# Kernel optimization log

Measured on AMD Instinct MI355X. Metric: run time of the kernel, lower is better.

The kernel has to match this reference:

```python
import jax, jax.numpy as jnp
import numpy as np

B, Q, D = 4, 8, 128  # batch of volumes, poses per volume, volume side (L == D)


def setup_inputs() -> dict:
    key = jax.random.key(0)
    k1, k2 = jax.random.split(key)
    density = jax.random.normal(k1, (B, D, D, D), dtype=jnp.float32)
    rotation = jax.random.normal(k2, (B, Q, 3, 3), dtype=jnp.float32)
    return {"density": density, "rotation": rotation}


def _project(density, rotation):
    """density: (B, NZ, NY, NX); rotation: (B, Q, 3, 3) -> (B, Q, NY, NX).

    Replicates: rotate an L^3 coord grid, F.grid_sample (trilinear,
    align_corners=True, zero padding), then sum over the last grid axis.
    """
    b, NZ, NY, NX = density.shape
    q = rotation.shape[1]
    L = NZ  # module asserts D == NZ == NY == NX and uses L == D

    lin = jnp.linspace(-1.0, 1.0, L, dtype=density.dtype)
    xx, yy, zz = jnp.meshgrid(lin, lin, lin, indexing="ij")
    coords = jnp.stack([xx, yy, zz], axis=-1)  # (L, L, L, 3)

    Rf = rotation.reshape(b * q, 3, 3)
    # rot_coords[n,i,j,k,m] = sum_c coords[i,j,k,c] * R[n,c,m]
    rc = jnp.einsum("ijkc,ncm->nijkm", coords, Rf)  # (BQ, L, L, L, 3)

    # grid_sample convention: last dim is (x, y, z) indexing (NX, NY, NZ).
    # align_corners=True unnormalization: idx = (c + 1) / 2 * (size - 1)
    x = (rc[..., 0] + 1.0) * 0.5 * (NX - 1)
    y = (rc[..., 1] + 1.0) * 0.5 * (NY - 1)
    z = (rc[..., 2] + 1.0) * 0.5 * (NZ - 1)

    x0 = jnp.floor(x).astype(jnp.int32)
    y0 = jnp.floor(y).astype(jnp.int32)
    z0 = jnp.floor(z).astype(jnp.int32)
    fx = x - x0
    fy = y - y0
    fz = z - z0

    vol = jnp.broadcast_to(density[:, None], (b, q, NZ, NY, NX))
    vol_flat = vol.reshape(b * q, NZ * NY * NX)

    def corner(xc, yc, zc, w):
        valid = (xc >= 0) & (xc < NX) & (yc >= 0) & (yc < NY) & (zc >= 0) & (zc < NZ)
        xi = jnp.clip(xc, 0, NX - 1)
        yi = jnp.clip(yc, 0, NY - 1)
        zi = jnp.clip(zc, 0, NZ - 1)
        idx = (zi * NY + yi) * NX + xi  # (BQ, L, L, L)
        v = jnp.take_along_axis(vol_flat, idx.reshape(b * q, -1), axis=1)
        v = v.reshape(idx.shape)
        return jnp.where(valid, v, 0.0) * w

    sampled = (
        corner(x0,     y0,     z0,     (1 - fx) * (1 - fy) * (1 - fz))
        + corner(x0 + 1, y0,     z0,     fx * (1 - fy) * (1 - fz))
        + corner(x0,     y0 + 1, z0,     (1 - fx) * fy * (1 - fz))
        + corner(x0 + 1, y0 + 1, z0,     fx * fy * (1 - fz))
        + corner(x0,     y0,     z0 + 1, (1 - fx) * (1 - fy) * fz)
        + corner(x0 + 1, y0,     z0 + 1, fx * (1 - fy) * fz)
        + corner(x0,     y0 + 1, z0 + 1, (1 - fx) * fy * fz)
        + corner(x0 + 1, y0 + 1, z0 + 1, fx * fy * fz)
    )  # (BQ, L, L, L) over grid axes (X, Y, Z)

    sampled = sampled.reshape(b, q, L, L, L)
    proj = jnp.sum(sampled.transpose(0, 1, 3, 2, 4), axis=-1)  # (B, Q, L, L)
    return proj


def reference(density, rotation):
    return _project(density, rotation)
```

## Files before the change

### kernel.cpp

```cpp
#include <hip/hip_runtime.h>


#define LSZ 128
#define PACKED_BYTES ((size_t)4 * 128 * 128 * 128 * 8)

typedef float f2 __attribute__((ext_vector_type(2), aligned(4)));
typedef unsigned int u4v __attribute__((ext_vector_type(4), aligned(8)));

__device__ __forceinline__ float bl(unsigned int d) {
    return __uint_as_float(d << 16);
}
__device__ __forceinline__ float bh(unsigned int d) {
    return __uint_as_float(d & 0xffff0000u);
}
__device__ __forceinline__ unsigned int pk2(float lo, float hi) {
    unsigned int ul = __float_as_uint(lo), uh = __float_as_uint(hi);
    ul = (ul + 0x7fffu + ((ul >> 16) & 1u)) >> 16;
    uh = (uh + 0x7fffu + ((uh >> 16) & 1u)) >> 16;
    return ul | (uh << 16);
}

__global__ __launch_bounds__(256) void pack_kernel(
    const float* __restrict__ density, uint2* __restrict__ packed)
{
    const int t  = blockIdx.x * 256 + threadIdx.x;
    const int xq = (t & 31) << 2;
    const int y  = (t >> 5) & 127;
    const int z  = (t >> 12) & 127;
    const int b  = t >> 19;
    const float* __restrict__ v = density + ((size_t)b << 21);
    const int y1 = min(y + 1, 127), z1 = min(z + 1, 127);
    const float4 a0 = *(const float4*)(v + (z  << 14) + (y  << 7) + xq);
    const float4 a1 = *(const float4*)(v + (z  << 14) + (y1 << 7) + xq);
    const float4 c0 = *(const float4*)(v + (z1 << 14) + (y  << 7) + xq);
    const float4 c1 = *(const float4*)(v + (z1 << 14) + (y1 << 7) + xq);
    uint4 o0, o1;
    o0.x = pk2(a0.x, a1.x); o0.y = pk2(c0.x, c1.x);
    o0.z = pk2(a0.y, a1.y); o0.w = pk2(c0.y, c1.y);
    o1.x = pk2(a0.z, a1.z); o1.y = pk2(c0.z, c1.z);
    o1.z = pk2(a0.w, a1.w); o1.w = pk2(c0.w, c1.w);
    uint4* dst = (uint4*)(packed + ((size_t)b << 21) + (z << 14) + (y << 7) + xq);
    dst[0] = o0; dst[1] = o1;
}

#define FPREPI(S, kk) do {                                                    \
    const float kf_ = (float)min((kk), d);                                    \
    const float X_ = fmaf(kf_, R20, Ax);                                      \
    const float Y_ = fmaf(kf_, R21, Ay);                                      \
    const float Z_ = fmaf(kf_, R22, Az);                                      \
    const int ix_ = (int)X_;                                                  \
    const int iy_ = (int)Y_;                                                  \
    const int iz_ = (int)Z_;                                                  \
    fx##S = X_ - (float)ix_;                                                  \
    fy##S = Y_ - (float)iy_;                                                  \
    fz##S = Z_ - (float)iz_;                                                  \
    u##S = *(const u4v*)(vol2 + ((iz_ << 14) + (iy_ << 7) + ix_));            \
} while (0)

#define FCONSI(S) do {                                                        \
    const float gx0 = 1.0f - fx##S;                                           \
    const float gy0 = 1.0f - fy##S;                                           \
    const float gz0 = 1.0f - fz##S;                                           \
    const float c000 = bl(u##S.x), c010 = bh(u##S.x);                         \
    const float c001 = bl(u##S.y), c011 = bh(u##S.y);                         \
    const float c100 = bl(u##S.z), c110 = bh(u##S.z);                         \
    const float c101 = bl(u##S.w), c111 = bh(u##S.w);                         \
    const float s0_ = gy0   * fmaf(gx0, c000, fx##S * c100)                   \
                    + fy##S * fmaf(gx0, c010, fx##S * c110);                  \
    const float s1_ = gy0   * fmaf(gx0, c001, fx##S * c101)                   \
                    + fy##S * fmaf(gx0, c011, fx##S * c111);                  \
    acc = fmaf(gz0, s0_, fmaf(fz##S, s1_, acc));                              \
} while (0)

#define SPREP(S, kk) do {                                                     \
    const float kf_ = (float)(kk);                                            \
    const float X_ = fmaf(kf_, R20, Ax);                                      \
    const float Y_ = fmaf(kf_, R21, Ay);                                      \
    const float Z_ = fmaf(kf_, R22, Az);                                      \
    const int ix_ = (int)floorf(X_);                                          \
    const int iy_ = (int)floorf(Y_);                                          \
    const int iz_ = (int)floorf(Z_);                                          \
    const int ex_ = min(max(ix_, 0), 126);                                    \
    const int ey_ = min(max(iy_, 0), 126);                                    \
    const int ez_ = min(max(iz_, 0), 126);                                    \
    u##S = *(const u4v*)(vol2 + ((ez_ << 14) + (ey_ << 7) + ex_));            \
} while (0)

#define SCONS(S, kk) do {                                                     \
    const float kf_ = (float)(kk);                                            \
    const float X_ = fmaf(kf_, R20, Ax);                                      \
    const float Y_ = fmaf(kf_, R21, Ay);                                      \
    const float Z_ = fmaf(kf_, R22, Az);                                      \
    const float xf_ = floorf(X_), yf_ = floorf(Y_), zf_ = floorf(Z_);         \
    const int ix_ = (int)xf_, iy_ = (int)yf_, iz_ = (int)zf_;                 \
    const float fx_ = X_ - xf_, fy_ = Y_ - yf_, fz_ = Z_ - zf_;               \
    const bool vx0_ = (ix_ >= 0)  & (ix_ <= 127);                             \
    const bool vx1_ = (ix_ >= -1) & (ix_ <= 126);                             \
    const bool vy0_ = (iy_ >= 0)  & (iy_ <= 127);                             \
    const bool vy1_ = (iy_ >= -1) & (iy_ <= 126);                             \
    const bool vz0_ = (iz_ >= 0)  & (iz_ <= 127);                             \
    const bool vz1_ = (iz_ >= -1) & (iz_ <= 126);                             \
    const float gx0 = vx0_ ? (1.0f - fx_) : 0.0f;                             \
    const float gx1 = vx1_ ? fx_ : 0.0f;                                      \
    const float gy0 = vy0_ ? (1.0f - fy_) : 0.0f;                             \
    const float gy1 = vy1_ ? fy_ : 0.0f;                                      \
    const float gz0 = vz0_ ? (1.0f - fz_) : 0.0f;                             \
    const float gz1 = vz1_ ? fz_ : 0.0f;                                      \
    const bool xhi_ = (ix_ > 126), xlo_ = (ix_ < 0);                          \
    const bool yhi_ = (iy_ > 126), ylo_ = (iy_ < 0);                          \
    const bool zhi_ = (iz_ > 126), zlo_ = (iz_ < 0);                          \
    const unsigned int a0z0 = xhi_ ? u##S.z : u##S.x;                         \
    const unsigned int a0z1 = xhi_ ? u##S.w : u##S.y;                         \
    const unsigned int a1z0 = xlo_ ? u##S.x : u##S.z;                         \
    const unsigned int a1z1 = xlo_ ? u##S.y : u##S.w;                         \
    const unsigned int dA = zhi_ ? a0z1 : a0z0;                               \
    const unsigned int dB = zlo_ ? a0z0 : a0z1;                               \
    const unsigned int dC = zhi_ ? a1z1 : a1z0;                               \
    const unsigned int dD = zlo_ ? a1z0 : a1z1;                               \
    const float c000 = yhi_ ? bh(dA) : bl(dA);                                \
    const float c010 = ylo_ ? bl(dA) : bh(dA);                                \
    const float c100 = yhi_ ? bh(dC) : bl(dC);                                \
    const float c110 = ylo_ ? bl(dC) : bh(dC);                                \
    const float c001 = yhi_ ? bh(dB) : bl(dB);                                \
    const float c011 = ylo_ ? bl(dB) : bh(dB);                                \
    const float c101 = yhi_ ? bh(dD) : bl(dD);                                \
    const float c111 = ylo_ ? bl(dD) : bh(dD);                                \
    const float s0_ = gy0 * fmaf(gx0, c000, gx1 * c100)                       \
                    + gy1 * fmaf(gx0, c010, gx1 * c110);                      \
    const float s1_ = gy0 * fmaf(gx0, c001, gx1 * c101)                       \
                    + gy1 * fmaf(gx0, c011, gx1 * c111);                      \
    acc = fmaf(gz0, s0_, fmaf(gz1, s1_, acc));                                \
} while (0)

__global__ __launch_bounds__(256) void proj_kernel_packed(
    const uint2* __restrict__ packed,
    const float* __restrict__ rotation,
    float* __restrict__ out)
{
    const int xcd  = blockIdx.x & 7;
    const int slot = blockIdx.x >> 3;
    const int b    = xcd >> 1;
    const int tile = ((xcd & 1) << 8) + slot;
    const int q    = tile >> 6;
    const int blk  = tile & 63;
    const int bq   = (b << 3) + q;

    const int p = (blk << 8) + threadIdx.x;
    const int i = p & (LSZ - 1);
    const int j = p >> 7;

    const float* R = rotation + bq * 9;
    const float R00 = R[0], R01 = R[1], R02 = R[2];
    const float R10 = R[3], R11 = R[4], R12 = R[5];
    const float R20 = R[6], R21 = R[7], R22 = R[8];

    const float step = 2.0f / 127.0f;
    const float li = -1.0f + (float)i * step;
    const float lj = -1.0f + (float)j * step;

    const float Ax = 63.5f * (li * R00 + lj * R10 - R20 + 1.0f);
    const float Ay = 63.5f * (li * R01 + lj * R11 - R21 + 1.0f);
    const float Az = 63.5f * (li * R02 + lj * R12 - R22 + 1.0f);

    float klo = 0.0f, khi = 127.0f;
    float klo2 = 0.0f, khi2 = 127.0f;
    bool empty = false, empty2 = false;
    {
        const float a_[3] = {Ax, Ay, Az};
        const float s_[3] = {R20, R21, R22};
        #pragma unroll
        for (int m = 0; m < 3; ++m) {
            if (fabsf(s_[m]) > 1e-6f) {
                const float r = 1.0f / s_[m];
                const float t0 = (-1.0f   - a_[m]) * r;
                const float t1 = (128.0f  - a_[m]) * r;
                klo = fmaxf(klo, fminf(t0, t1));
                khi = fminf(khi, fmaxf(t0, t1));
                const float w0 = (0.0f    - a_[m]) * r;
                const float w1 = (126.95f - a_[m]) * r;
                klo2 = fmaxf(klo2, fminf(w0, w1));
                khi2 = fminf(khi2, fmaxf(w0, w1));
            } else {
                if (a_[m] <= -1.0f   || a_[m] >= 128.0f)   empty  = true;
                if (a_[m] <  0.001f  || a_[m] >  126.94f)  empty2 = true;
            }
        }
    }
    int a = (int)ceilf(klo - 1e-3f);
    int bnd = (int)floorf(khi + 1e-3f);
    if (a < 0) a = 0;
    if (bnd > 127) bnd = 127;
    if (empty) bnd = a - 1;

    int c = (int)ceilf(klo2 + 0.05f);
    int d = (int)floorf(khi2 - 0.05f);
    if (c < a) c = a;
    if (d > bnd) d = bnd;
    if (empty2 || d < c) { c = bnd + 1; d = bnd; }

    const uint2* __restrict__ vol2 = packed + ((size_t)b << 21);

    float acc = 0.0f;
    u4v uA, uB, uC, uD;
    float fxA, fyA, fzA, fxB, fyB, fzB, fxC, fyC, fzC, fxD, fyD, fzD;

    {
        int k = a;
        const int e = c - 1;
        if (k <= e) {
            SPREP(A, k);
            while (k <= e) {
                const int kn = k + 1;
                const bool hasB = (kn <= e);
                if (hasB) SPREP(B, kn);
                SCONS(A, k);
                if (hasB) SCONS(B, kn);
                k += 2;
                if (k <= e) SPREP(A, k);
            }
        }
    }

    {
        int n = d - c + 1;
        int k = c;
        if (n > 0) {
            FPREPI(A, k); FPREPI(B, k + 1); FPREPI(C, k + 2);
            while (n > 0) {
                FPREPI(D, k + 3);
                FCONSI(A);
                FPREPI(A, k + 4);
                if (n > 1) FCONSI(B);
                FPREPI(B, k + 5);
                if (n > 2) FCONSI(C);
                FPREPI(C, k + 6);
                if (n > 3) FCONSI(D);
                k += 4; n -= 4;
            }
        }
    }

    {
        int k = d + 1;
        const int e = bnd;
        if (k <= e) {
            SPREP(A, k);
            while (k <= e) {
                const int kn = k + 1;
                const bool hasB = (kn <= e);
                if (hasB) SPREP(B, kn);
                SCONS(A, k);
                if (hasB) SCONS(B, kn);
                k += 2;
                if (k <= e) SPREP(A, k);
            }
        }
    }

    out[(bq << 14) + p] = acc;
}

__global__ __launch_bounds__(256) void proj_kernel_fallback(
    const float* __restrict__ density,
    const float* __restrict__ rotation,
    float* __restrict__ out)
{
    const int xcd  = blockIdx.x & 7;
    const int slot = blockIdx.x >> 3;
    const int b    = xcd >> 1;
    const int tile = ((xcd & 1) << 8) + slot;
    const int q    = tile >> 6;
    const int blk  = tile & 63;
    const int bq   = (b << 3) + q;

    const int p = (blk << 8) + threadIdx.x;
    const int i = p & (LSZ - 1);
    const int j = p >> 7;

    const float* R = rotation + bq * 9;
    const float R00 = R[0], R01 = R[1], R02 = R[2];
    const float R10 = R[3], R11 = R[4], R12 = R[5];
    const float R20 = R[6], R21 = R[7], R22 = R[8];

    const float step = 2.0f / 127.0f;
    const float li = -1.0f + (float)i * step;
    const float lj = -1.0f + (float)j * step;

    const float Ax = 63.5f * (li * R00 + lj * R10 - R20 + 1.0f);
    const float Ay = 63.5f * (li * R01 + lj * R11 - R21 + 1.0f);
    const float Az = 63.5f * (li * R02 + lj * R12 - R22 + 1.0f);

    float klo = 0.0f, khi = 127.0f;
    bool empty = false;
    {
        const float a_[3] = {Ax, Ay, Az};
        const float s_[3] = {R20, R21, R22};
        #pragma unroll
        for (int m = 0; m < 3; ++m) {
            if (fabsf(s_[m]) > 1e-6f) {
                const float t0 = (-1.0f  - a_[m]) / s_[m];
                const float t1 = (128.0f - a_[m]) / s_[m];
                klo = fmaxf(klo, fminf(t0, t1));
                khi = fminf(khi, fmaxf(t0, t1));
            } else if (a_[m] <= -1.0f || a_[m] >= 128.0f) {
                empty = true;
            }
        }
    }
    int k_start = (int)ceilf(klo - 1e-3f);
    int k_end   = (int)floorf(khi + 1e-3f);
    if (k_start < 0) k_start = 0;
    if (k_end > 127) k_end = 127;
    if (empty) k_end = k_start - 1;

    const float* __restrict__ vol = density + (size_t)b * (LSZ * LSZ * LSZ);

    float acc = 0.0f;
    for (int k = k_start; k <= k_end; ++k) {
        const float kf = (float)k;
        const float X = fmaf(kf, R20, Ax);
        const float Y = fmaf(kf, R21, Ay);
        const float Z = fmaf(kf, R22, Az);
        const float xf = floorf(X), yf = floorf(Y), zf = floorf(Z);
        const int ix = (int)xf, iy = (int)yf, iz = (int)zf;
        const float fx = X - xf, fy = Y - yf, fz = Z - zf;
        const bool vx0 = (ix >= 0)  & (ix <= 127);
        const bool vx1 = (ix >= -1) & (ix <= 126);
        const bool vy0 = (iy >= 0)  & (iy <= 127);
        const bool vy1 = (iy >= -1) & (iy <= 126);
        const bool vz0 = (iz >= 0)  & (iz <= 127);
        const bool vz1 = (iz >= -1) & (iz <= 126);
        const int cx0 = min(max(ix, 0), 127);
        const int cx1 = min(max(ix + 1, 0), 127);
        const int cy0 = min(max(iy, 0), 127);
        const int cy1 = min(max(iy + 1, 0), 127);
        const int cz0 = min(max(iz, 0), 127);
        const int cz1 = min(max(iz + 1, 0), 127);
        const float gx0 = vx0 ? (1.0f - fx) : 0.0f;
        const float gx1 = vx1 ? fx : 0.0f;
        const float gy0 = vy0 ? (1.0f - fy) : 0.0f;
        const float gy1 = vy1 ? fy : 0.0f;
        const float gz0 = vz0 ? (1.0f - fz) : 0.0f;
        const float gz1 = vz1 ? fz : 0.0f;
        const int z0o = cz0 << 14, z1o = cz1 << 14;
        const int y0o = cy0 << 7,  y1o = cy1 << 7;
        const float v000 = vol[z0o + y0o + cx0];
        const float v100 = vol[z0o + y0o + cx1];
        const float v010 = vol[z0o + y1o + cx0];
        const float v110 = vol[z0o + y1o + cx1];
        const float v001 = vol[z1o + y0o + cx0];
        const float v101 = vol[z1o + y0o + cx1];
        const float v011 = vol[z1o + y1o + cx0];
        const float v111 = vol[z1o + y1o + cx1];
        const float s0 = gy0 * fmaf(gx0, v000, gx1 * v100)
                       + gy1 * fmaf(gx0, v010, gx1 * v110);
        const float s1 = gy0 * fmaf(gx0, v001, gx1 * v101)
                       + gy1 * fmaf(gx0, v011, gx1 * v111);
        acc = fmaf(gz0, s0, fmaf(gz1, s1, acc));
    }

    out[(bq << 14) + p] = acc;
}

extern "C" void kernel_launch(void* const* d_in, const int* in_sizes, int n_in,
                              void* d_out, int out_size, void* d_ws, size_t ws_size,
                              hipStream_t stream) {
    const float* density  = (const float*)d_in[0];
    const float* rotation = (const float*)d_in[1];
    float* out = (float*)d_out;

    if (ws_size >= PACKED_BYTES) {
        uint2* packed = (uint2*)d_ws;
        pack_kernel<<<8192, 256, 0, stream>>>(density, packed);
        proj_kernel_packed<<<2048, 256, 0, stream>>>(packed, rotation, out);
    } else {
        proj_kernel_fallback<<<2048, 256, 0, stream>>>(density, rotation, out);
    }
}
```

Baseline: 204.6 us.

## Pack volume as fp16 pairs and use dot2 for y-interpolation with deeper prefetch

The packed volume switches from bf16 to fp16 pairs. Each y-interpolation pair of corners is reduced with a single v_dot2 instruction using packed (1-fy, fy) weights, which removes the bf16 unpacking and several FMAs per sample. The interior loop's software pipeline grows from 4 to 6 in-flight gathers, with a remainder tail, and fract builtins compute the fractional parts. In exchange, fp16 has a narrower range and round-toward-zero conversion of weights and data, which may hurt accuracy. The extra in-flight loads also raise register pressure.

```diff
diff --git a/kernel.cpp b/kernel.cpp
--- a/kernel.cpp
+++ b/kernel.cpp
@@ -4,20 +4,22 @@
 #define LSZ 128
 #define PACKED_BYTES ((size_t)4 * 128 * 128 * 128 * 8)
 
-typedef float f2 __attribute__((ext_vector_type(2), aligned(4)));
 typedef unsigned int u4v __attribute__((ext_vector_type(4), aligned(8)));
-
-__device__ __forceinline__ float bl(unsigned int d) {
-    return __uint_as_float(d << 16);
-}
-__device__ __forceinline__ float bh(unsigned int d) {
-    return __uint_as_float(d & 0xffff0000u);
-}
-__device__ __forceinline__ unsigned int pk2(float lo, float hi) {
-    unsigned int ul = __float_as_uint(lo), uh = __float_as_uint(hi);
-    ul = (ul + 0x7fffu + ((ul >> 16) & 1u)) >> 16;
-    uh = (uh + 0x7fffu + ((uh >> 16) & 1u)) >> 16;
-    return ul | (uh << 16);
+typedef _Float16 h2 __attribute__((ext_vector_type(2)));
+
+__device__ __forceinline__ h2 ash2(unsigned int u) {
+    union { unsigned int u; h2 h; } c; c.u = u; return c.h;
+}
+__device__ __forceinline__ float dot2(unsigned int pair, h2 w, float acc) {
+    return __builtin_amdgcn_fdot2(ash2(pair), w, acc, false);
+}
+__device__ __forceinline__ h2 pkw(float lo, float hi) {
+    auto t = __builtin_amdgcn_cvt_pkrtz(lo, hi);
+    union { decltype(t) a; h2 b; } c; c.a = t; return c.b;
+}
+__device__ __forceinline__ unsigned int pkh(float lo, float hi) {
+    auto t = __builtin_amdgcn_cvt_pkrtz(lo, hi);
+    union { decltype(t) a; unsigned int u; } c; c.a = t; return c.u;
 }
 
 __global__ __launch_bounds__(256) void pack_kernel(
@@ -35,10 +37,10 @@
     const float4 c0 = *(const float4*)(v + (z1 << 14) + (y  << 7) + xq);
     const float4 c1 = *(const float4*)(v + (z1 << 14) + (y1 << 7) + xq);
     uint4 o0, o1;
-    o0.x = pk2(a0.x, a1.x); o0.y = pk2(c0.x, c1.x);
-    o0.z = pk2(a0.y, a1.y); o0.w = pk2(c0.y, c1.y);
-    o1.x = pk2(a0.z, a1.z); o1.y = pk2(c0.z, c1.z);
-    o1.z = pk2(a0.w, a1.w); o1.w = pk2(c0.w, c1.w);
+    o0.x = pkh(a0.x, a1.x); o0.y = pkh(c0.x, c1.x);
+    o0.z = pkh(a0.y, a1.y); o0.w = pkh(c0.y, c1.y);
+    o1.x = pkh(a0.z, a1.z); o1.y = pkh(c0.z, c1.z);
+    o1.z = pkh(a0.w, a1.w); o1.w = pkh(c0.w, c1.w);
     uint4* dst = (uint4*)(packed + ((size_t)b << 21) + (z << 14) + (y << 7) + xq);
     dst[0] = o0; dst[1] = o1;
 }
@@ -51,24 +53,22 @@
     const int ix_ = (int)X_;                                                  \
     const int iy_ = (int)Y_;                                                  \
     const int iz_ = (int)Z_;                                                  \
-    fx##S = X_ - (float)ix_;                                                  \
-    fy##S = Y_ - (float)iy_;                                                  \
-    fz##S = Z_ - (float)iz_;                                                  \
+    fx##S = __builtin_amdgcn_fractf(X_);                                      \
+    const float fy_ = __builtin_amdgcn_fractf(Y_);                            \
+    fz##S = __builtin_amdgcn_fractf(Z_);                                      \
+    hy##S = pkw(1.0f - fy_, fy_);                                             \
     u##S = *(const u4v*)(vol2 + ((iz_ << 14) + (iy_ << 7) + ix_));            \
 } while (0)
 
 #define FCONSI(S) do {                                                        \
     const float gx0 = 1.0f - fx##S;                                           \
-    const float gy0 = 1.0f - fy##S;                                           \
     const float gz0 = 1.0f - fz##S;                                           \
-    const float c000 = bl(u##S.x), c010 = bh(u##S.x);                         \
-    const float c001 = bl(u##S.y), c011 = bh(u##S.y);                         \
-    const float c100 = bl(u##S.z), c110 = bh(u##S.z);                         \
-    const float c101 = bl(u##S.w), c111 = bh(u##S.w);                         \
-    const float s0_ = gy0   * fmaf(gx0, c000, fx##S * c100)                   \
-                    + fy##S * fmaf(gx0, c010, fx##S * c110);                  \
-    const float s1_ = gy0   * fmaf(gx0, c001, fx##S * c101)                   \
-                    + fy##S * fmaf(gx0, c011, fx##S * c111);                  \
+    const float m00 = dot2(u##S.x, hy##S, 0.0f);                 \
+    const float m01 = dot2(u##S.y, hy##S, 0.0f);                 \
+    const float m10 = dot2(u##S.z, hy##S, 0.0f);                 \
+    const float m11 = dot2(u##S.w, hy##S, 0.0f);                 \
+    const float s0_ = fmaf(gx0, m00, fx##S * m10);                            \
+    const float s1_ = fmaf(gx0, m01, fx##S * m11);                            \
     acc = fmaf(gz0, s0_, fmaf(fz##S, s1_, acc));                              \
 } while (0)
 
@@ -109,26 +109,23 @@
     const bool xhi_ = (ix_ > 126), xlo_ = (ix_ < 0);                          \
     const bool yhi_ = (iy_ > 126), ylo_ = (iy_ < 0);                          \
     const bool zhi_ = (iz_ > 126), zlo_ = (iz_ < 0);                          \
+    const float wlo_ = ylo_ ? gy1 : (yhi_ ? 0.0f : gy0);                      \
+    const float whi_ = yhi_ ? gy0 : (ylo_ ? 0.0f : gy1);                      \
+    const h2 hy_ = pkw(wlo_, whi_);                                           \
     const unsigned int a0z0 = xhi_ ? u##S.z : u##S.x;                         \
     const unsigned int a0z1 = xhi_ ? u##S.w : u##S.y;                         \
     const unsigned int a1z0 = xlo_ ? u##S.x : u##S.z;                         \
     const unsigned int a1z1 = xlo_ ? u##S.y : u##S.w;                         \
-    const unsigned int dA = zhi_ ? a0z1 : a0z0;                               \
-    const unsigned int dB = zlo_ ? a0z0 : a0z1;                               \
-    const unsigned int dC = zhi_ ? a1z1 : a1z0;                               \
-    const unsigned int dD = zlo_ ? a1z0 : a1z1;                               \
-    const float c000 = yhi_ ? bh(dA) : bl(dA);                                \
-    const float c010 = ylo_ ? bl(dA) : bh(dA);                                \
-    const float c100 = yhi_ ? bh(dC) : bl(dC);                                \
-    const float c110 = ylo_ ? bl(dC) : bh(dC);                                \
-    const float c001 = yhi_ ? bh(dB) : bl(dB);                                \
-    const float c011 = ylo_ ? bl(dB) : bh(dB);                                \
-    const float c101 = yhi_ ? bh(dD) : bl(dD);                                \
-    const float c111 = ylo_ ? bl(dD) : bh(dD);                                \
-    const float s0_ = gy0 * fmaf(gx0, c000, gx1 * c100)                       \
-                    + gy1 * fmaf(gx0, c010, gx1 * c110);                      \
-    const float s1_ = gy0 * fmaf(gx0, c001, gx1 * c101)                       \
-                    + gy1 * fmaf(gx0, c011, gx1 * c111);                      \
+    const unsigned int dA = zhi_ ? a0z1 : a0z0;                  \
+    const unsigned int dB = zlo_ ? a0z0 : a0z1;                  \
+    const unsigned int dC = zhi_ ? a1z1 : a1z0;                  \
+    const unsigned int dD = zlo_ ? a1z0 : a1z1;                  \
+    const float m00 = dot2(dA, hy_, 0.0f);                                    \
+    const float m01 = dot2(dB, hy_, 0.0f);                                    \
+    const float m10 = dot2(dC, hy_, 0.0f);                                    \
+    const float m11 = dot2(dD, hy_, 0.0f);                                    \
+    const float s0_ = fmaf(gx0, m00, gx1 * m10);                              \
+    const float s1_ = fmaf(gx0, m01, gx1 * m11);                              \
     acc = fmaf(gz0, s0_, fmaf(gz1, s1_, acc));                                \
 } while (0)
 
@@ -201,8 +198,10 @@
     const uint2* __restrict__ vol2 = packed + ((size_t)b << 21);
 
     float acc = 0.0f;
-    u4v uA, uB, uC, uD;
-    float fxA, fyA, fzA, fxB, fyB, fzB, fxC, fyC, fzC, fxD, fyD, fzD;
+    u4v uA, uB, uC, uD, uE, uF;
+    h2 hyA, hyB, hyC, hyD, hyE, hyF;
+    float fxA, fzA, fxB, fzB, fxC, fzC, fxD, fzD, fxE, fzE, fxF, fzF;
+    (void)hyA; (void)fxA; (void)fzA;
 
     {
         int k = a;
@@ -225,18 +224,23 @@
         int n = d - c + 1;
         int k = c;
         if (n > 0) {
-            FPREPI(A, k); FPREPI(B, k + 1); FPREPI(C, k + 2);
-            while (n > 0) {
-                FPREPI(D, k + 3);
-                FCONSI(A);
-                FPREPI(A, k + 4);
-                if (n > 1) FCONSI(B);
-                FPREPI(B, k + 5);
-                if (n > 2) FCONSI(C);
-                FPREPI(C, k + 6);
-                if (n > 3) FCONSI(D);
-                k += 4; n -= 4;
-            }
+            FPREPI(A, k);     FPREPI(B, k + 1); FPREPI(C, k + 2);
+            FPREPI(D, k + 3); FPREPI(E, k + 4);
+            while (n >= 6) {
+                FPREPI(F, k + 5);
+                FCONSI(A); FPREPI(A, k + 6);
+                FCONSI(B); FPREPI(B, k + 7);
+                FCONSI(C); FPREPI(C, k + 8);
+                FCONSI(D); FPREPI(D, k + 9);
+                FCONSI(E); FPREPI(E, k + 10);
+                FCONSI(F);
+                k += 6; n -= 6;
+            }
+            if (n > 0) FCONSI(A);
+            if (n > 1) FCONSI(B);
+            if (n > 2) FCONSI(C);
+            if (n > 3) FCONSI(D);
+            if (n > 4) FCONSI(E);
         }
     }
 
```

Result: slower. 213.1 us (+4.2%).
